# Kernel optimization log

Hardware: AMD Instinct MI355X
Metric: run time of the kernel (lower is better)

The kernel has to match this reference:

```python
import jax, jax.numpy as jnp
import numpy as np

B, Lq, C, NH, NP, DFF = 8, 10000, 256, 8, 4, 1024
H_IMG, W_IMG = 100, 100
HD = C // NH


def _layer_norm(x, g, b, eps=1e-5):
    m = jnp.mean(x, -1, keepdims=True)
    v = jnp.mean((x - m) ** 2, -1, keepdims=True)
    return (x - m) / jnp.sqrt(v + eps) * g + b


def _bilinear_sample(value, loc, Hs, Ws):
    # value: [B, Lin, NH, HD]; loc: [B, Lq, NH, NP, 2] normalized to [0,1]
    vt = jnp.transpose(value, (0, 2, 1, 3))  # [B, NH, Lin, HD]
    # move to [B, NH, Lq, NP] layout once; grid_sample(align_corners=False) pixel coords
    x = jnp.transpose(loc[..., 0], (0, 2, 1, 3)) * Ws - 0.5
    y = jnp.transpose(loc[..., 1], (0, 2, 1, 3)) * Hs - 0.5
    x0 = jnp.floor(x); y0 = jnp.floor(y)
    lx = x - x0; ly = y - y0

    def corner(xi, yi, w):
        valid = (xi >= 0) & (xi < Ws) & (yi >= 0) & (yi < Hs)
        xc = jnp.clip(xi, 0, Ws - 1).astype(jnp.int32)
        yc = jnp.clip(yi, 0, Hs - 1).astype(jnp.int32)
        idx = (yc * Ws + xc).reshape(B, NH, Lq * NP, 1)
        v = jnp.take_along_axis(vt, idx, axis=2).reshape(B, NH, Lq, NP, HD)
        return v * (w * valid)[..., None]

    acc = corner(x0, y0, (1 - lx) * (1 - ly))
    acc = acc + corner(x0 + 1, y0, lx * (1 - ly))
    acc = acc + corner(x0, y0 + 1, (1 - lx) * ly)
    acc = acc + corner(x0 + 1, y0 + 1, lx * ly)
    return acc  # [B, NH, Lq, NP, HD]


def setup_inputs() -> dict:
    key = jax.random.key(0)
    ks = jax.random.split(key, 12)
    s = 0.02
    return {
        "query": jax.random.normal(ks[0], (B, Lq, C), jnp.float32),
        "src": jax.random.normal(ks[1], (B, H_IMG * W_IMG, C), jnp.float32),
        "reference_points": jax.random.uniform(ks[2], (B, Lq, 1, 2), jnp.float32),
        "spatial_shapes": jnp.array([[H_IMG, W_IMG]], dtype=jnp.int64),
        "level_start_index": jnp.array([0], dtype=jnp.int64),
        "W_off": jax.random.normal(ks[3], (C, NH * NP * 2), jnp.float32) * s,
        "b_off": jnp.zeros((NH * NP * 2,), jnp.float32),
        "W_aw": jax.random.normal(ks[4], (C, NH * NP), jnp.float32) * s,
        "b_aw": jnp.zeros((NH * NP,), jnp.float32),
        "W_val": jax.random.normal(ks[5], (C, C), jnp.float32) * s,
        "b_val": jnp.zeros((C,), jnp.float32),
        "W_out": jax.random.normal(ks[6], (C, C), jnp.float32) * s,
        "b_out": jnp.zeros((C,), jnp.float32),
        "g1": jnp.ones((C,), jnp.float32),
        "be1": jnp.zeros((C,), jnp.float32),
        "W1": jax.random.normal(ks[7], (C, DFF), jnp.float32) * s,
        "b1": jnp.zeros((DFF,), jnp.float32),
        "W2": jax.random.normal(ks[8], (DFF, C), jnp.float32) * s,
        "b2": jnp.zeros((C,), jnp.float32),
        "g2": jnp.ones((C,), jnp.float32),
        "be2": jnp.zeros((C,), jnp.float32),
    }


def reference(query, src, reference_points, spatial_shapes, level_start_index,
              W_off, b_off, W_aw, b_aw, W_val, b_val, W_out, b_out,
              g1, be1, W1, b1, W2, b2, g2, be2):
    Hs = spatial_shapes[0, 0]
    Ws = spatial_shapes[0, 1]
    # MSDeformAttn (n_levels = 1)
    value = (src @ W_val + b_val).reshape(B, -1, NH, HD)
    off = (query @ W_off + b_off).reshape(B, Lq, NH, NP, 2)
    aw = jax.nn.softmax((query @ W_aw + b_aw).reshape(B, Lq, NH, NP), axis=-1)
    normalizer = jnp.stack([Ws, Hs]).astype(query.dtype)  # (W, H)
    loc = reference_points[:, :, None] + off / normalizer  # [B,Lq,NH,NP,2]
    sampled = _bilinear_sample(value, loc, Hs, Ws)  # [B,NH,Lq,NP,HD]
    attn = jnp.einsum('bhqpd,bqhp->bqhd', sampled, aw).reshape(B, Lq, C)
    attn = attn @ W_out + b_out
    # residual + LN + FFN + LN
    q = _layer_norm(query + attn, g1, be1)
    ffn = jax.nn.relu(q @ W1 + b1) @ W2 + b2
    return _layer_norm(q + ffn, g2, be2)
```

## Files before the change

kernel.cpp:

```cpp
#include <hip/hip_runtime.h>
#include <hip/hip_bf16.h>

typedef __hip_bfloat16 bf16;
typedef unsigned short u16;
typedef short short8 __attribute__((ext_vector_type(8)));
typedef float f32x4 __attribute__((ext_vector_type(4)));

static constexpr int B_   = 8;
static constexpr int Lq_  = 10000;
static constexpr int C_   = 256;
static constexpr int NH_  = 8;
static constexpr int NP_  = 4;
static constexpr int HIMG = 100;
static constexpr int WIMG = 100;
static constexpr int LIN  = 10000;

__device__ __forceinline__ u16 f2bf(float x) {
    union { bf16 b; u16 u; } cv; cv.b = __float2bfloat16(x); return cv.u;
}
__device__ __forceinline__ float bf2f(u16 u) {
    return __uint_as_float((unsigned)u << 16);
}

__device__ __forceinline__ void gl_lds16(const void* g, void* l) {
    __builtin_amdgcn_global_load_lds(
        (const __attribute__((address_space(1))) void*)g,
        (__attribute__((address_space(3))) void*)l, 16, 0, 0);
}
__device__ __forceinline__ void drain_barrier() {
    asm volatile("s_waitcnt vmcnt(0) lgkmcnt(0)" ::: "memory");
    __builtin_amdgcn_s_barrier();
}
#define VMW(N) asm volatile("s_waitcnt vmcnt(" #N ")" ::: "memory")
#define LKW0() asm volatile("s_waitcnt lgkmcnt(0)" ::: "memory")
#define BAR()  __builtin_amdgcn_s_barrier()

template <bool AF32, bool LN>
__global__ __launch_bounds__(512, 2) void gemm256(
    const void* __restrict__ Av, const u16* __restrict__ Bg,
    const float* __restrict__ bias, const float* __restrict__ resid,
    const float* __restrict__ gw, const float* __restrict__ bw,
    u16* __restrict__ Co, int K)
{
    __shared__ __align__(16) u16 At[2][128 * 64];
    __shared__ __align__(16) u16 Bt[2][256 * 64];
    __shared__ float red[2][128][4];

    const int tid  = threadIdx.x;
    const int lane = tid & 63;
    const int w    = tid >> 6;
    const int wm   = w >> 2, wn = w & 3;
    const int m0   = blockIdx.x * 128;

    f32x4 acc[4][4];
#pragma unroll
    for (int i = 0; i < 4; ++i)
#pragma unroll
        for (int j = 0; j < 4; ++j) acc[i][j] = f32x4{0.f, 0.f, 0.f, 0.f};

    auto stageA = [&](int t) {
        const int kt = t << 6;
        if constexpr (AF32) {
            const int row = tid >> 2;
            const int k0  = (tid & 3) << 4;
            const float* s = (const float*)Av + (size_t)(m0 + row) * K + kt + k0;
            float4 v0 = *(const float4*)(s + 0);
            float4 v1 = *(const float4*)(s + 4);
            float4 v2 = *(const float4*)(s + 8);
            float4 v3 = *(const float4*)(s + 12);
            union { short8 s8; u16 u[8]; } ga, gb;
            ga.u[0]=f2bf(v0.x); ga.u[1]=f2bf(v0.y); ga.u[2]=f2bf(v0.z); ga.u[3]=f2bf(v0.w);
            ga.u[4]=f2bf(v1.x); ga.u[5]=f2bf(v1.y); ga.u[6]=f2bf(v1.z); ga.u[7]=f2bf(v1.w);
            gb.u[0]=f2bf(v2.x); gb.u[1]=f2bf(v2.y); gb.u[2]=f2bf(v2.z); gb.u[3]=f2bf(v2.w);
            gb.u[4]=f2bf(v3.x); gb.u[5]=f2bf(v3.y); gb.u[6]=f2bf(v3.z); gb.u[7]=f2bf(v3.w);
            u16* d = &At[t & 1][row * 64];
            *(short8*)&d[(k0)     ^ ((row & 7) << 3)] = ga.s8;
            *(short8*)&d[(k0 + 8) ^ ((row & 7) << 3)] = gb.s8;
        } else {
#pragma unroll
            for (int i = 0; i < 2; ++i) {
                const int rb  = w * 16 + i * 8;
                const int row = rb + (lane >> 3);
                const int gs  = (lane & 7) ^ (row & 7);
                gl_lds16((const u16*)Av + (size_t)(m0 + row) * K + kt + gs * 8,
                         &At[t & 1][rb * 64]);
            }
        }
    };
    auto stageB = [&](int t) {
        const int kt = t << 6;
#pragma unroll
        for (int i = 0; i < 4; ++i) {
            const int rb  = w * 32 + i * 8;
            const int row = rb + (lane >> 3);
            gl_lds16(Bg + (size_t)row * K + kt + (lane & 7) * 8,
                     &Bt[t & 1][rb * 64]);
        }
    };
    auto compute = [&](int t) {
        const u16* a = At[t & 1];
        const u16* b = Bt[t & 1];
#pragma unroll
        for (int ks = 0; ks < 2; ++ks) {
            const int ko = ks * 32 + ((lane >> 4) << 3);
            short8 bfr[4];
#pragma unroll
            for (int n = 0; n < 4; ++n) {
                const int nr = wn * 64 + n * 16 + (lane & 15);
                bfr[n] = *(const short8*)&b[nr * 64 + (ko ^ ((nr & 7) << 3))];
            }
#pragma unroll
            for (int m = 0; m < 4; ++m) {
                const int ar = wm * 64 + m * 16 + (lane & 15);
                const short8 af = *(const short8*)&a[ar * 64 + (ko ^ ((ar & 7) << 3))];
#pragma unroll
                for (int n = 0; n < 4; ++n)
                    acc[m][n] = __builtin_amdgcn_mfma_f32_16x16x32_bf16(
                        af, bfr[n], acc[m][n], 0, 0, 0);
            }
        }
    };

    stageA(0); stageB(0);
    drain_barrier();
    const int nt = K >> 6;
    for (int t = 0; t < nt; ++t) {
        if (t + 1 < nt) { stageA(t + 1); stageB(t + 1); }
        compute(t);
        drain_barrier();
    }

    float bcol[4], gcol[4], becol[4];
#pragma unroll
    for (int n = 0; n < 4; ++n) {
        const int col = wn * 64 + n * 16 + (lane & 15);
        bcol[n] = bias[col];
        if (LN) { gcol[n] = gw[col]; becol[n] = bw[col]; }
    }

    if constexpr (!LN) {
#pragma unroll
        for (int m = 0; m < 4; ++m)
#pragma unroll
            for (int r = 0; r < 4; ++r) {
                const int lr = wm * 64 + m * 16 + (lane >> 4) * 4 + r;
#pragma unroll
                for (int n = 0; n < 4; ++n) {
                    const int col = wn * 64 + n * 16 + (lane & 15);
                    Co[(size_t)(m0 + lr) * 256 + col] = f2bf(acc[m][n][r] + bcol[n]);
                }
            }
    } else {
        float s[4][4], s2[4][4];
#pragma unroll
        for (int m = 0; m < 4; ++m)
#pragma unroll
            for (int r = 0; r < 4; ++r) {
                const int lr = wm * 64 + m * 16 + (lane >> 4) * 4 + r;
                float ps = 0.f, ps2 = 0.f;
#pragma unroll
                for (int n = 0; n < 4; ++n) {
                    const int col = wn * 64 + n * 16 + (lane & 15);
                    float v = acc[m][n][r] + bcol[n]
                            + resid[(size_t)(m0 + lr) * 256 + col];
                    acc[m][n][r] = v;
                    ps += v; ps2 += v * v;
                }
#pragma unroll
                for (int o = 1; o < 16; o <<= 1) {
                    ps  += __shfl_xor(ps,  o);
                    ps2 += __shfl_xor(ps2, o);
                }
                s[m][r] = ps; s2[m][r] = ps2;
            }
        if ((lane & 15) == 0) {
#pragma unroll
            for (int m = 0; m < 4; ++m)
#pragma unroll
                for (int r = 0; r < 4; ++r) {
                    const int lr = wm * 64 + m * 16 + (lane >> 4) * 4 + r;
                    red[0][lr][wn] = s[m][r];
                    red[1][lr][wn] = s2[m][r];
                }
        }
        __syncthreads();
        if (tid < 128) {
            const float ss  = red[0][tid][0] + red[0][tid][1] + red[0][tid][2] + red[0][tid][3];
            const float ss2 = red[1][tid][0] + red[1][tid][1] + red[1][tid][2] + red[1][tid][3];
            const float mean = ss * (1.f / 256.f);
            const float var  = fmaxf(ss2 * (1.f / 256.f) - mean * mean, 0.f);
            red[0][tid][0] = mean;
            red[1][tid][0] = rsqrtf(var + 1e-5f);
        }
        __syncthreads();
#pragma unroll
        for (int m = 0; m < 4; ++m)
#pragma unroll
            for (int r = 0; r < 4; ++r) {
                const int lr = wm * 64 + m * 16 + (lane >> 4) * 4 + r;
                const float mean = red[0][lr][0];
                const float rstd = red[1][lr][0];
#pragma unroll
                for (int n = 0; n < 4; ++n) {
                    const int col = wn * 64 + n * 16 + (lane & 15);
                    const float o = (acc[m][n][r] - mean) * rstd * gcol[n] + becol[n];
                    Co[(size_t)(m0 + lr) * 256 + (col ^ ((lr & 7) << 3))] = f2bf(o);
                }
            }
    }
}

__global__ __launch_bounds__(512) void ffn_fused(
    const u16* __restrict__ q1b, const u16* __restrict__ W1t,
    const u16* __restrict__ W2t, const float* __restrict__ b1,
    const float* __restrict__ b2, const float* __restrict__ g2w,
    const float* __restrict__ be2, float* __restrict__ out)
{
    __shared__ __align__(16) u16 As[128 * 256];
    __shared__ __align__(16) u16 Hs[128 * 136];
    __shared__ __align__(16) u16 B1s[3][4096];
    __shared__ __align__(16) u16 B2s[3][4096];
    float (*red)[128][4] = (float (*)[128][4])Hs;

    const int tid  = threadIdx.x;
    const int lane = tid & 63;
    const int w    = tid >> 6;
    const int wm   = w >> 2, wn = w & 3;
    const int m0   = blockIdx.x * 128;
    const int ko   = (lane >> 4) << 3;

    int bfb[2];
#pragma unroll
    for (int q = 0; q < 2; ++q) {
        const int nr = wn * 32 + q * 16 + (lane & 15);
        const int pr = nr >> 1;
        bfb[q] = pr * 64 + (nr & 1) * 32 + (ko ^ ((pr & 3) << 3));
    }
    int arow[4], aswz[4], hrow[4];
#pragma unroll
    for (int m = 0; m < 4; ++m) {
        const int ar = wm * 64 + m * 16 + (lane & 15);
        arow[m] = ar * 256; aswz[m] = (ar & 7) << 3; hrow[m] = ar * 136;
    }

    f32x4 acc2[4][4];
#pragma unroll
    for (int i = 0; i < 4; ++i)
#pragma unroll
        for (int j = 0; j < 4; ++j) acc2[i][j] = f32x4{0.f, 0.f, 0.f, 0.f};

    auto issueB1 = [&](int tile, int buf) {
        gl_lds16(W1t + (size_t)tile * 4096 + w * 512 + lane * 8, &B1s[buf][w * 512]);
    };
    auto issueB2 = [&](int tile, int buf) {
        gl_lds16(W2t + (size_t)tile * 4096 + w * 512 + lane * 8, &B2s[buf][w * 512]);
    };

#pragma unroll
    for (int i = 0; i < 8; ++i) {
        const int rb = w * 16 + i * 2;
        gl_lds16(q1b + (size_t)(m0 + rb + (lane >> 5)) * 256 + (lane & 31) * 8,
                 &As[rb * 256]);
    }
    issueB1(0, 0); issueB1(1, 1);
    VMW(1); BAR();

    for (int c = 0; c < 8; ++c) {
        const int bb = c * 8;
        f32x4 acc1[4][2];
#pragma unroll
        for (int i = 0; i < 4; ++i)
#pragma unroll
            for (int j = 0; j < 2; ++j) acc1[i][j] = f32x4{0.f, 0.f, 0.f, 0.f};

        auto g1 = [&](int t, int buf) {
            short8 bfr[2];
#pragma unroll
            for (int q = 0; q < 2; ++q)
                bfr[q] = *(const short8*)&B1s[buf][bfb[q]];
            __builtin_amdgcn_s_setprio(1);
#pragma unroll
            for (int m = 0; m < 4; ++m) {
                const short8 af = *(const short8*)
                    &As[arow[m] + ((t * 32 + ko) ^ aswz[m])];
#pragma unroll
                for (int q = 0; q < 2; ++q)
                    acc1[m][q] = __builtin_amdgcn_mfma_f32_16x16x32_bf16(
                        af, bfr[q], acc1[m][q], 0, 0, 0);
            }
            __builtin_amdgcn_s_setprio(0);
        };

#pragma unroll
        for (int t = 0; t < 6; ++t) {
            issueB1(bb + t + 2, (bb + t + 2) % 3);
            g1(t, (bb + t) % 3);
            VMW(1); BAR();
        }
        issueB2(bb + 0, (bb + 0) % 3); g1(6, (bb + 6) % 3); VMW(1); BAR();
        issueB2(bb + 1, (bb + 1) % 3); g1(7, (bb + 7) % 3); VMW(1); BAR();

#pragma unroll
        for (int q = 0; q < 2; ++q) {
            const int col = wn * 32 + q * 16 + (lane & 15);
            const float bv = b1[c * 128 + col];
#pragma unroll
            for (int m = 0; m < 4; ++m)
#pragma unroll
                for (int r = 0; r < 4; ++r) {
                    const int row = wm * 64 + m * 16 + (lane >> 4) * 4 + r;
                    Hs[row * 136 + col] = f2bf(fmaxf(acc1[m][q][r] + bv, 0.f));
                }
        }
        LKW0(); BAR();

#pragma unroll
        for (int j = 0; j < 6; ++j) {
            issueB2(bb + j + 2, (bb + j + 2) % 3);
            {
                const int ku = j >> 1, nh = j & 1;
                short8 bfr[2];
#pragma unroll
                for (int q = 0; q < 2; ++q)
                    bfr[q] = *(const short8*)&B2s[(bb + j) % 3][bfb[q]];
                __builtin_amdgcn_s_setprio(1);
#pragma unroll
                for (int m = 0; m < 4; ++m) {
                    const short8 af = *(const short8*)&Hs[hrow[m] + ku * 32 + ko];
#pragma unroll
                    for (int q = 0; q < 2; ++q)
                        acc2[m][2 * nh + q] = __builtin_amdgcn_mfma_f32_16x16x32_bf16(
                            af, bfr[q], acc2[m][2 * nh + q], 0, 0, 0);
                }
                __builtin_amdgcn_s_setprio(0);
            }
            VMW(1); BAR();
        }
#pragma unroll
        for (int j = 6; j < 8; ++j) {
            issueB1(c < 7 ? bb + 8 + (j - 6) : (j - 6), (bb + 8 + (j - 6)) % 3);
            {
                const int ku = j >> 1, nh = j & 1;
                short8 bfr[2];
#pragma unroll
                for (int q = 0; q < 2; ++q)
                    bfr[q] = *(const short8*)&B2s[(bb + j) % 3][bfb[q]];
                __builtin_amdgcn_s_setprio(1);
#pragma unroll
                for (int m = 0; m < 4; ++m) {
                    const short8 af = *(const short8*)&Hs[hrow[m] + ku * 32 + ko];
#pragma unroll
                    for (int q = 0; q < 2; ++q)
                        acc2[m][2 * nh + q] = __builtin_amdgcn_mfma_f32_16x16x32_bf16(
                            af, bfr[q], acc2[m][2 * nh + q], 0, 0, 0);
                }
                __builtin_amdgcn_s_setprio(0);
            }
            VMW(1); BAR();
        }
    }
    asm volatile("s_waitcnt vmcnt(0)" ::: "memory");
    BAR();

    float bcol[4], gcol[4], becol[4];
#pragma unroll
    for (int n = 0; n < 4; ++n) {
        const int col = wn * 64 + n * 16 + (lane & 15);
        bcol[n] = b2[col]; gcol[n] = g2w[col]; becol[n] = be2[col];
    }
    float s[4][4], s2[4][4];
#pragma unroll
    for (int m = 0; m < 4; ++m)
#pragma unroll
        for (int r = 0; r < 4; ++r) {
            const int lr = wm * 64 + m * 16 + (lane >> 4) * 4 + r;
            float ps = 0.f, ps2 = 0.f;
#pragma unroll
            for (int n = 0; n < 4; ++n) {
                const int col = wn * 64 + n * 16 + (lane & 15);
                const float q = bf2f(As[lr * 256 + (col ^ ((lr & 7) << 3))]);
                const float v = acc2[m][n][r] + bcol[n] + q;
                acc2[m][n][r] = v;
                ps += v; ps2 += v * v;
            }
#pragma unroll
            for (int o = 1; o < 16; o <<= 1) {
                ps  += __shfl_xor(ps,  o);
                ps2 += __shfl_xor(ps2, o);
            }
            s[m][r] = ps; s2[m][r] = ps2;
        }
    if ((lane & 15) == 0) {
#pragma unroll
        for (int m = 0; m < 4; ++m)
#pragma unroll
            for (int r = 0; r < 4; ++r) {
                const int lr = wm * 64 + m * 16 + (lane >> 4) * 4 + r;
                red[0][lr][wn] = s[m][r];
                red[1][lr][wn] = s2[m][r];
            }
    }
    __syncthreads();
    if (tid < 128) {
        const float ss  = red[0][tid][0] + red[0][tid][1] + red[0][tid][2] + red[0][tid][3];
        const float ss2 = red[1][tid][0] + red[1][tid][1] + red[1][tid][2] + red[1][tid][3];
        const float mean = ss * (1.f / 256.f);
        const float var  = fmaxf(ss2 * (1.f / 256.f) - mean * mean, 0.f);
        red[0][tid][0] = mean;
        red[1][tid][0] = rsqrtf(var + 1e-5f);
    }
    __syncthreads();
#pragma unroll
    for (int m = 0; m < 4; ++m)
#pragma unroll
        for (int r = 0; r < 4; ++r) {
            const int lr = wm * 64 + m * 16 + (lane >> 4) * 4 + r;
            const float mean = red[0][lr][0];
            const float rstd = red[1][lr][0];
#pragma unroll
            for (int n = 0; n < 4; ++n) {
                const int col = wn * 64 + n * 16 + (lane & 15);
                out[(size_t)(m0 + lr) * 256 + col] =
                    (acc2[m][n][r] - mean) * rstd * gcol[n] + becol[n];
            }
        }
}

__global__ __launch_bounds__(256) void gemm_oaw(
    const float* __restrict__ Av, const u16* __restrict__ Bt,
    const float* __restrict__ bias, float* __restrict__ C,
    int M, int K, int Nreal, int ldc)
{
    __shared__ __align__(16) u16 Asl[2][128 * 32];
    __shared__ __align__(16) u16 Bsl[2][128 * 32];

    const int tid  = threadIdx.x;
    const int lane = tid & 63;
    const int w    = tid >> 6;
    const int wr   = (w >> 1) * 64;
    const int wc   = (w & 1) * 64;
    const int m0   = blockIdx.y * 128;
    const int n0   = blockIdx.x * 128;

    const int srow = lane >> 2;
    const int scol = (lane & 3) << 3;
    const u16* bG = Bt + (size_t)(n0 + w * 32 + srow) * K + scol;
    const size_t rstep16 = (size_t)16 * K;

    const int ar  = lane >> 3;
    const int ac  = (lane & 7) << 2;
    const float* aGf = Av + (size_t)(m0 + w * 32 + ar) * K + ac;

    const int aRoff = (wr + (lane & 15)) * 32 + (lane >> 4) * 8;
    const int bRoff = (wc + (lane & 15)) * 32 + (lane >> 4) * 8;

    f32x4 acc[4][4];
#pragma unroll
    for (int i = 0; i < 4; ++i)
#pragma unroll
        for (int j = 0; j < 4; ++j) acc[i][j] = f32x4{0.f, 0.f, 0.f, 0.f};

    float4 a4[4];
    const int nt = K >> 5;

#pragma unroll
    for (int rep = 0; rep < 4; ++rep)
        a4[rep] = *(const float4*)(aGf + (size_t)(rep * 8) * K);
#pragma unroll
    for (int rep = 0; rep < 4; ++rep) {
        ushort4 v{f2bf(a4[rep].x), f2bf(a4[rep].y), f2bf(a4[rep].z), f2bf(a4[rep].w)};
        *(ushort4*)&Asl[0][(w * 32 + rep * 8 + ar) * 32 + ac] = v;
    }
    gl_lds16(bG, &Bsl[0][(w * 32) * 32]);
    gl_lds16(bG + rstep16, &Bsl[0][(w * 32 + 16) * 32]);
    drain_barrier();

    for (int t = 0; t < nt; ++t) {
        const int cur = t & 1, nxt = cur ^ 1;
        const int k0n = (t + 1) << 5;
        const bool has_next = (t + 1 < nt);
        if (has_next) {
#pragma unroll
            for (int rep = 0; rep < 4; ++rep)
                a4[rep] = *(const float4*)(aGf + k0n + (size_t)(rep * 8) * K);
            gl_lds16(bG + k0n, &Bsl[nxt][(w * 32) * 32]);
            gl_lds16(bG + k0n + rstep16, &Bsl[nxt][(w * 32 + 16) * 32]);
        }
        short8 af[4], bfr[4];
#pragma unroll
        for (int m = 0; m < 4; ++m) af[m]  = *(const short8*)&Asl[cur][aRoff + m * 16 * 32];
#pragma unroll
        for (int n = 0; n < 4; ++n) bfr[n] = *(const short8*)&Bsl[cur][bRoff + n * 16 * 32];
#pragma unroll
        for (int m = 0; m < 4; ++m)
#pragma unroll
            for (int n = 0; n < 4; ++n)
                acc[m][n] = __builtin_amdgcn_mfma_f32_16x16x32_bf16(
                    af[m], bfr[n], acc[m][n], 0, 0, 0);
        if (has_next) {
#pragma unroll
            for (int rep = 0; rep < 4; ++rep) {
                ushort4 v{f2bf(a4[rep].x), f2bf(a4[rep].y), f2bf(a4[rep].z), f2bf(a4[rep].w)};
                *(ushort4*)&Asl[nxt][(w * 32 + rep * 8 + ar) * 32 + ac] = v;
            }
        }
        drain_barrier();
    }

#pragma unroll
    for (int n = 0; n < 4; ++n) {
        const int gc = n0 + wc + n * 16 + (lane & 15);
        if (gc >= Nreal) continue;
        const float bv = bias[gc];
        const int gr0 = m0 + wr + (lane >> 4) * 4;
#pragma unroll
        for (int m = 0; m < 4; ++m)
#pragma unroll
            for (int r = 0; r < 4; ++r)
                C[(size_t)(gr0 + m * 16 + r) * ldc + gc] = acc[m][n][r] + bv;
    }
}

__global__ __launch_bounds__(256) void prep_all(
    const float* __restrict__ Wv, const float* __restrict__ Wo,
    const float* __restrict__ W1, const float* __restrict__ W2,
    const float* __restrict__ Woff, const float* __restrict__ Waw,
    const float* __restrict__ boff, const float* __restrict__ baw,
    u16* __restrict__ Wvs, u16* __restrict__ Wos,
    u16* __restrict__ W1t, u16* __restrict__ W2t,
    u16* __restrict__ Woa, float* __restrict__ boa)
{
    const int idx = blockIdx.x * 256 + threadIdx.x;
    if (idx < 65536) {
        const int n = idx >> 8, kd = idx & 255;
        Wvs[idx] = f2bf(Wv[(size_t)(kd ^ ((n & 7) << 3)) * 256 + n]);
    } else if (idx < 131072) {
        const int i = idx - 65536, n = i >> 8, kd = i & 255;
        Wos[i] = f2bf(Wo[(size_t)(kd ^ ((n & 7) << 3)) * 256 + n]);
    } else if (idx < 393216) {
        const int i = idx - 131072;
        const int tile = i >> 12, si = i & 4095;
        const int c = tile >> 3, t = tile & 7;
        const int pr = si >> 6, inner = si & 63;
        const int nr = (pr << 1) | (inner >> 5);
        const int kk = (inner & 31) ^ ((pr & 3) << 3);
        W1t[i] = f2bf(W1[(size_t)(t * 32 + kk) * 1024 + c * 128 + nr]);
    } else if (idx < 655360) {
        const int i = idx - 393216;
        const int tile = i >> 12, si = i & 4095;
        const int c = tile >> 3, j = tile & 7;
        const int ku = j >> 1, nh = j & 1;
        const int pr = si >> 6, inner = si & 63;
        const int rl = (pr << 1) | (inner >> 5);
        const int kk = (inner & 31) ^ ((pr & 3) << 3);
        const int n = ((rl >> 5) << 6) + (nh << 5) + (rl & 31);
        W2t[i] = f2bf(W2[(size_t)(c * 128 + ku * 32 + kk) * 256 + n]);
    } else if (idx < 688128) {
        const int i = idx - 655360, n = i >> 8, k = i & 255;
        float v = 0.f;
        if (n < 64)      v = Woff[(size_t)k * 64 + n];
        else if (n < 96) v = Waw[(size_t)k * 32 + (n - 64)];
        Woa[i] = f2bf(v);
    } else if (idx < 688256) {
        const int i = idx - 688128;
        boa[i] = (i < 64) ? boff[i] : (i < 96 ? baw[i - 64] : 0.f);
    }
}

__global__ __launch_bounds__(256) void sample_attn(
    const u16* __restrict__ val, const float* __restrict__ oaw,
    const float* __restrict__ refp, u16* __restrict__ attn)
{
    const int t   = threadIdx.x;
    const int gid = blockIdx.x * 64 + (t >> 2);
    const int c0  = (t & 3) << 3;
    const int h   = gid & (NH_ - 1);
    const int bq  = gid >> 3;

    const float* row = oaw + (size_t)bq * 96;
    const float rx = refp[(size_t)bq * 2 + 0] * (float)WIMG;
    const float ry = refp[(size_t)bq * 2 + 1] * (float)HIMG;

    const float4 aw4 = *(const float4*)(row + 64 + h * 4);
    const float mx = fmaxf(fmaxf(aw4.x, aw4.y), fmaxf(aw4.z, aw4.w));
    const float e0 = __expf(aw4.x - mx), e1 = __expf(aw4.y - mx);
    const float e2 = __expf(aw4.z - mx), e3 = __expf(aw4.w - mx);
    const float inv = 1.f / (e0 + e1 + e2 + e3);
    const float w4[4] = {e0 * inv, e1 * inv, e2 * inv, e3 * inv};

    const int b = bq / Lq_;
    const u16* vb = val + (size_t)b * LIN * C_ + h * 32 + c0;

    float acc[8] = {};
#pragma unroll
    for (int p = 0; p < NP_; ++p) {
        const float2 off = *(const float2*)(row + (h * 4 + p) * 2);
        const float x = rx + off.x - 0.5f;
        const float y = ry + off.y - 0.5f;
        const float xf = floorf(x), yf = floorf(y);
        const float lx = x - xf, ly = y - yf;
        const int x0 = (int)xf, y0 = (int)yf;
        const float wp = w4[p];
        const float w00 = wp * (1.f - lx) * (1.f - ly);
        const float w10 = wp * lx * (1.f - ly);
        const float w01 = wp * (1.f - lx) * ly;
        const float w11 = wp * lx * ly;

#pragma unroll
        for (int c = 0; c < 4; ++c) {
            const int xi = x0 + (c & 1);
            const int yi = y0 + (c >> 1);
            const float wc = (c == 0) ? w00 : (c == 1) ? w10 : (c == 2) ? w01 : w11;
            const bool v = ((unsigned)xi < (unsigned)WIMG) & ((unsigned)yi < (unsigned)HIMG);
            const int idx = v ? (yi * WIMG + xi) : 0;
            const float w = v ? wc : 0.f;
            const short8 d = *(const short8*)(vb + (size_t)idx * C_);
#pragma unroll
            for (int j = 0; j < 8; ++j)
                acc[j] = fmaf(w, bf2f(((const u16*)&d)[j]), acc[j]);
        }
    }

    union { short8 s; u16 u[8]; } o;
#pragma unroll
    for (int j = 0; j < 8; ++j) o.u[j] = f2bf(acc[j]);
    *(short8*)(attn + (size_t)bq * C_ + h * 32 + c0) = o.s;
}

extern "C" void kernel_launch(void* const* d_in, const int* in_sizes, int n_in,
                              void* d_out, int out_size, void* d_ws, size_t ws_size,
                              hipStream_t stream)
{
    const float* query = (const float*)d_in[0];
    const float* src   = (const float*)d_in[1];
    const float* refp  = (const float*)d_in[2];
    const float* W_off = (const float*)d_in[5];
    const float* b_off = (const float*)d_in[6];
    const float* W_aw  = (const float*)d_in[7];
    const float* b_aw  = (const float*)d_in[8];
    const float* W_val = (const float*)d_in[9];
    const float* b_val = (const float*)d_in[10];
    const float* W_out = (const float*)d_in[11];
    const float* b_out = (const float*)d_in[12];
    const float* g1    = (const float*)d_in[13];
    const float* be1   = (const float*)d_in[14];
    const float* W1    = (const float*)d_in[15];
    const float* b1    = (const float*)d_in[16];
    const float* W2    = (const float*)d_in[17];
    const float* b2    = (const float*)d_in[18];
    const float* g2    = (const float*)d_in[19];
    const float* be2   = (const float*)d_in[20];
    float* out = (float*)d_out;

    char* ws = (char*)d_ws;
    const int R = B_ * Lq_;

    u16*  val  = (u16*)(ws + 0);
    float* oaw = (float*)(ws + 40960000);
    u16*  attn = (u16*)(ws + 71680000);
    u16*  q1b  = (u16*)(ws + 112640000);
    u16*  Wvs  = (u16*)(ws + 153600000);
    u16*  Wos  = (u16*)(ws + 153600000 + 131072);
    u16*  W1t  = (u16*)(ws + 153600000 + 262144);
    u16*  W2t  = (u16*)(ws + 153600000 + 786432);
    u16*  Woa  = (u16*)(ws + 153600000 + 1310720);
    float* boa = (float*)(ws + 153600000 + 1376256);

    prep_all<<<2689, 256, 0, stream>>>(W_val, W_out, W1, W2, W_off, W_aw,
                                       b_off, b_aw, Wvs, Wos, W1t, W2t,
                                       Woa, boa);

    gemm256<true, false><<<625, 512, 0, stream>>>(
        src, Wvs, b_val, nullptr, nullptr, nullptr, val, 256);

    gemm_oaw<<<dim3(1, 625), 256, 0, stream>>>(
        query, Woa, boa, oaw, R, 256, 96, 96);

    sample_attn<<<10000, 256, 0, stream>>>(val, oaw, refp, attn);

    gemm256<false, true><<<625, 512, 0, stream>>>(
        attn, Wos, b_out, query, g1, be1, q1b, 256);

    ffn_fused<<<625, 512, 0, stream>>>(q1b, W1t, W2t, b1, b2, g2, be2, out);
}
```

Baseline: 374.3 us.

## Retile fused FFN to 64-row blocks with double-buffered weight staging

The fused FFN kernel moves from 128-row tiles with 512 threads to 64-row tiles with 256 threads, launched as 1250 blocks. The triple-buffered, partially waited weight pipeline becomes a double buffer with a full drain barrier after each k-step. The hidden tile gets an XOR swizzle in place of padding, and the W2 prepack layout changes to match the new per-wave column split. Shared-memory use drops so more blocks can fit on a CU and the 1250 blocks spread more evenly across CUs. In exchange, each weight tile is fetched twice as often per output row, the load/compute overlap is coarser, and the MFMA priority hints are gone.

```diff
diff --git a/kernel.cpp b/kernel.cpp
--- a/kernel.cpp
+++ b/kernel.cpp
@@ -31,9 +31,6 @@
     asm volatile("s_waitcnt vmcnt(0) lgkmcnt(0)" ::: "memory");
     __builtin_amdgcn_s_barrier();
 }
-#define VMW(N) asm volatile("s_waitcnt vmcnt(" #N ")" ::: "memory")
-#define LKW0() asm volatile("s_waitcnt lgkmcnt(0)" ::: "memory")
-#define BAR()  __builtin_amdgcn_s_barrier()
 
 template <bool AF32, bool LN>
 __global__ __launch_bounds__(512, 2) void gemm256(
@@ -210,50 +207,57 @@
     }
 }
 
-__global__ __launch_bounds__(512) void ffn_fused(
+__global__ __launch_bounds__(256) void ffn_fused(
     const u16* __restrict__ q1b, const u16* __restrict__ W1t,
     const u16* __restrict__ W2t, const float* __restrict__ b1,
     const float* __restrict__ b2, const float* __restrict__ g2w,
     const float* __restrict__ be2, float* __restrict__ out)
 {
-    __shared__ __align__(16) u16 As[128 * 256];
-    __shared__ __align__(16) u16 Hs[128 * 136];
-    __shared__ __align__(16) u16 B1s[3][4096];
-    __shared__ __align__(16) u16 B2s[3][4096];
-    float (*red)[128][4] = (float (*)[128][4])Hs;
+    __shared__ __align__(16) u16 As[64 * 256];
+    __shared__ __align__(16) u16 Hs[64 * 128];
+    __shared__ __align__(16) u16 B1s[2][4096];
+    __shared__ __align__(16) u16 B2s[2][4096];
+    float (*red)[64][2] = (float (*)[64][2])Hs;
 
     const int tid  = threadIdx.x;
     const int lane = tid & 63;
     const int w    = tid >> 6;
-    const int wm   = w >> 2, wn = w & 3;
-    const int m0   = blockIdx.x * 128;
+    const int wm   = w >> 1, wn = w & 1;
+    const int m0   = blockIdx.x * 64;
     const int ko   = (lane >> 4) << 3;
 
-    int bfb[2];
-#pragma unroll
-    for (int q = 0; q < 2; ++q) {
-        const int nr = wn * 32 + q * 16 + (lane & 15);
+    int bfb[4];
+#pragma unroll
+    for (int q = 0; q < 4; ++q) {
+        const int nr = wn * 64 + q * 16 + (lane & 15);
         const int pr = nr >> 1;
         bfb[q] = pr * 64 + (nr & 1) * 32 + (ko ^ ((pr & 3) << 3));
     }
-    int arow[4], aswz[4], hrow[4];
-#pragma unroll
-    for (int m = 0; m < 4; ++m) {
-        const int ar = wm * 64 + m * 16 + (lane & 15);
-        arow[m] = ar * 256; aswz[m] = (ar & 7) << 3; hrow[m] = ar * 136;
-    }
-
-    f32x4 acc2[4][4];
-#pragma unroll
-    for (int i = 0; i < 4; ++i)
-#pragma unroll
-        for (int j = 0; j < 4; ++j) acc2[i][j] = f32x4{0.f, 0.f, 0.f, 0.f};
-
-    auto issueB1 = [&](int tile, int buf) {
-        gl_lds16(W1t + (size_t)tile * 4096 + w * 512 + lane * 8, &B1s[buf][w * 512]);
+    int arow[2], aswz[2], hrow[2], hswz[2];
+#pragma unroll
+    for (int m = 0; m < 2; ++m) {
+        const int ar = wm * 32 + m * 16 + (lane & 15);
+        arow[m] = ar * 256; aswz[m] = (ar & 7) << 3;
+        hrow[m] = ar * 128; hswz[m] = (ar & 7) << 3;
+    }
+
+    f32x4 acc2[2][8];
+#pragma unroll
+    for (int i = 0; i < 2; ++i)
+#pragma unroll
+        for (int j = 0; j < 8; ++j) acc2[i][j] = f32x4{0.f, 0.f, 0.f, 0.f};
+
+    auto stageB1 = [&](int tile, int buf) {
+#pragma unroll
+        for (int i = 0; i < 2; ++i)
+            gl_lds16(W1t + (size_t)tile * 4096 + w * 1024 + i * 512 + lane * 8,
+                     &B1s[buf][w * 1024 + i * 512]);
     };
-    auto issueB2 = [&](int tile, int buf) {
-        gl_lds16(W2t + (size_t)tile * 4096 + w * 512 + lane * 8, &B2s[buf][w * 512]);
+    auto stageB2 = [&](int tile, int buf) {
+#pragma unroll
+        for (int i = 0; i < 2; ++i)
+            gl_lds16(W2t + (size_t)tile * 4096 + w * 1024 + i * 512 + lane * 8,
+                     &B2s[buf][w * 1024 + i * 512]);
     };
 
 #pragma unroll
@@ -262,125 +266,92 @@
         gl_lds16(q1b + (size_t)(m0 + rb + (lane >> 5)) * 256 + (lane & 31) * 8,
                  &As[rb * 256]);
     }
-    issueB1(0, 0); issueB1(1, 1);
-    VMW(1); BAR();
+    stageB1(0, 0);
+    drain_barrier();
 
     for (int c = 0; c < 8; ++c) {
-        const int bb = c * 8;
-        f32x4 acc1[4][2];
-#pragma unroll
-        for (int i = 0; i < 4; ++i)
-#pragma unroll
-            for (int j = 0; j < 2; ++j) acc1[i][j] = f32x4{0.f, 0.f, 0.f, 0.f};
-
-        auto g1 = [&](int t, int buf) {
-            short8 bfr[2];
-#pragma unroll
-            for (int q = 0; q < 2; ++q)
-                bfr[q] = *(const short8*)&B1s[buf][bfb[q]];
-            __builtin_amdgcn_s_setprio(1);
-#pragma unroll
-            for (int m = 0; m < 4; ++m) {
+        f32x4 acc1[2][4];
+#pragma unroll
+        for (int i = 0; i < 2; ++i)
+#pragma unroll
+            for (int j = 0; j < 4; ++j) acc1[i][j] = f32x4{0.f, 0.f, 0.f, 0.f};
+
+#pragma unroll
+        for (int t = 0; t < 8; ++t) {
+            if (t < 7) stageB1(c * 8 + t + 1, (t + 1) & 1);
+            else       stageB2(c * 8 + 0, 0);
+            short8 bfr[4];
+#pragma unroll
+            for (int q = 0; q < 4; ++q)
+                bfr[q] = *(const short8*)&B1s[t & 1][bfb[q]];
+#pragma unroll
+            for (int m = 0; m < 2; ++m) {
                 const short8 af = *(const short8*)
                     &As[arow[m] + ((t * 32 + ko) ^ aswz[m])];
 #pragma unroll
-                for (int q = 0; q < 2; ++q)
+                for (int q = 0; q < 4; ++q)
                     acc1[m][q] = __builtin_amdgcn_mfma_f32_16x16x32_bf16(
                         af, bfr[q], acc1[m][q], 0, 0, 0);
             }
-            __builtin_amdgcn_s_setprio(0);
-        };
-
-#pragma unroll
-        for (int t = 0; t < 6; ++t) {
-            issueB1(bb + t + 2, (bb + t + 2) % 3);
-            g1(t, (bb + t) % 3);
-            VMW(1); BAR();
-        }
-        issueB2(bb + 0, (bb + 0) % 3); g1(6, (bb + 6) % 3); VMW(1); BAR();
-        issueB2(bb + 1, (bb + 1) % 3); g1(7, (bb + 7) % 3); VMW(1); BAR();
-
-#pragma unroll
-        for (int q = 0; q < 2; ++q) {
-            const int col = wn * 32 + q * 16 + (lane & 15);
+            drain_barrier();
+        }
+
+#pragma unroll
+        for (int q = 0; q < 4; ++q) {
+            const int col = wn * 64 + q * 16 + (lane & 15);
             const float bv = b1[c * 128 + col];
 #pragma unroll
-            for (int m = 0; m < 4; ++m)
+            for (int m = 0; m < 2; ++m)
 #pragma unroll
                 for (int r = 0; r < 4; ++r) {
-                    const int row = wm * 64 + m * 16 + (lane >> 4) * 4 + r;
-                    Hs[row * 136 + col] = f2bf(fmaxf(acc1[m][q][r] + bv, 0.f));
+                    const int row = wm * 32 + m * 16 + (lane >> 4) * 4 + r;
+                    Hs[row * 128 + (col ^ ((row & 7) << 3))] =
+                        f2bf(fmaxf(acc1[m][q][r] + bv, 0.f));
                 }
         }
-        LKW0(); BAR();
-
-#pragma unroll
-        for (int j = 0; j < 6; ++j) {
-            issueB2(bb + j + 2, (bb + j + 2) % 3);
-            {
-                const int ku = j >> 1, nh = j & 1;
-                short8 bfr[2];
-#pragma unroll
-                for (int q = 0; q < 2; ++q)
-                    bfr[q] = *(const short8*)&B2s[(bb + j) % 3][bfb[q]];
-                __builtin_amdgcn_s_setprio(1);
-#pragma unroll
-                for (int m = 0; m < 4; ++m) {
-                    const short8 af = *(const short8*)&Hs[hrow[m] + ku * 32 + ko];
-#pragma unroll
-                    for (int q = 0; q < 2; ++q)
-                        acc2[m][2 * nh + q] = __builtin_amdgcn_mfma_f32_16x16x32_bf16(
-                            af, bfr[q], acc2[m][2 * nh + q], 0, 0, 0);
-                }
-                __builtin_amdgcn_s_setprio(0);
-            }
-            VMW(1); BAR();
-        }
-#pragma unroll
-        for (int j = 6; j < 8; ++j) {
-            issueB1(c < 7 ? bb + 8 + (j - 6) : (j - 6), (bb + 8 + (j - 6)) % 3);
-            {
-                const int ku = j >> 1, nh = j & 1;
-                short8 bfr[2];
-#pragma unroll
-                for (int q = 0; q < 2; ++q)
-                    bfr[q] = *(const short8*)&B2s[(bb + j) % 3][bfb[q]];
-                __builtin_amdgcn_s_setprio(1);
-#pragma unroll
-                for (int m = 0; m < 4; ++m) {
-                    const short8 af = *(const short8*)&Hs[hrow[m] + ku * 32 + ko];
-#pragma unroll
-                    for (int q = 0; q < 2; ++q)
-                        acc2[m][2 * nh + q] = __builtin_amdgcn_mfma_f32_16x16x32_bf16(
-                            af, bfr[q], acc2[m][2 * nh + q], 0, 0, 0);
-                }
-                __builtin_amdgcn_s_setprio(0);
-            }
-            VMW(1); BAR();
-        }
-    }
-    asm volatile("s_waitcnt vmcnt(0)" ::: "memory");
-    BAR();
-
-    float bcol[4], gcol[4], becol[4];
-#pragma unroll
-    for (int n = 0; n < 4; ++n) {
-        const int col = wn * 64 + n * 16 + (lane & 15);
-        bcol[n] = b2[col]; gcol[n] = g2w[col]; becol[n] = be2[col];
-    }
-    float s[4][4], s2[4][4];
-#pragma unroll
-    for (int m = 0; m < 4; ++m)
+        drain_barrier();
+
+#pragma unroll
+        for (int j = 0; j < 8; ++j) {
+            if (j < 7) stageB2(c * 8 + j + 1, (j + 1) & 1);
+            else       stageB1(c < 7 ? (c + 1) * 8 : 0, 0);
+            const int ku = j >> 1, nh = j & 1;
+            short8 bfr[4];
+#pragma unroll
+            for (int q = 0; q < 4; ++q)
+                bfr[q] = *(const short8*)&B2s[j & 1][bfb[q]];
+#pragma unroll
+            for (int m = 0; m < 2; ++m) {
+                const short8 af = *(const short8*)
+                    &Hs[hrow[m] + ((ku * 32 + ko) ^ hswz[m])];
+#pragma unroll
+                for (int q = 0; q < 4; ++q)
+                    acc2[m][nh * 4 + q] = __builtin_amdgcn_mfma_f32_16x16x32_bf16(
+                        af, bfr[q], acc2[m][nh * 4 + q], 0, 0, 0);
+            }
+            drain_barrier();
+        }
+    }
+
+    float bcol[8], gcol[8], becol[8];
+#pragma unroll
+    for (int nf = 0; nf < 8; ++nf) {
+        const int col = (nf >> 2) * 128 + wn * 64 + (nf & 3) * 16 + (lane & 15);
+        bcol[nf] = b2[col]; gcol[nf] = g2w[col]; becol[nf] = be2[col];
+    }
+    float s[2][4], s2[2][4];
+#pragma unroll
+    for (int m = 0; m < 2; ++m)
 #pragma unroll
         for (int r = 0; r < 4; ++r) {
-            const int lr = wm * 64 + m * 16 + (lane >> 4) * 4 + r;
+            const int lr = wm * 32 + m * 16 + (lane >> 4) * 4 + r;
             float ps = 0.f, ps2 = 0.f;
 #pragma unroll
-            for (int n = 0; n < 4; ++n) {
-                const int col = wn * 64 + n * 16 + (lane & 15);
+            for (int nf = 0; nf < 8; ++nf) {
+                const int col = (nf >> 2) * 128 + wn * 64 + (nf & 3) * 16 + (lane & 15);
                 const float q = bf2f(As[lr * 256 + (col ^ ((lr & 7) << 3))]);
-                const float v = acc2[m][n][r] + bcol[n] + q;
-                acc2[m][n][r] = v;
+                const float v = acc2[m][nf][r] + bcol[nf] + q;
+                acc2[m][nf][r] = v;
                 ps += v; ps2 += v * v;
             }
 #pragma unroll
@@ -392,18 +363,18 @@
         }
     if ((lane & 15) == 0) {
 #pragma unroll
-        for (int m = 0; m < 4; ++m)
+        for (int m = 0; m < 2; ++m)
 #pragma unroll
             for (int r = 0; r < 4; ++r) {
-                const int lr = wm * 64 + m * 16 + (lane >> 4) * 4 + r;
+                const int lr = wm * 32 + m * 16 + (lane >> 4) * 4 + r;
                 red[0][lr][wn] = s[m][r];
                 red[1][lr][wn] = s2[m][r];
             }
     }
     __syncthreads();
-    if (tid < 128) {
-        const float ss  = red[0][tid][0] + red[0][tid][1] + red[0][tid][2] + red[0][tid][3];
-        const float ss2 = red[1][tid][0] + red[1][tid][1] + red[1][tid][2] + red[1][tid][3];
+    if (tid < 64) {
+        const float ss  = red[0][tid][0] + red[0][tid][1];
+        const float ss2 = red[1][tid][0] + red[1][tid][1];
         const float mean = ss * (1.f / 256.f);
         const float var  = fmaxf(ss2 * (1.f / 256.f) - mean * mean, 0.f);
         red[0][tid][0] = mean;
@@ -411,17 +382,17 @@
     }
     __syncthreads();
 #pragma unroll
-    for (int m = 0; m < 4; ++m)
+    for (int m = 0; m < 2; ++m)
 #pragma unroll
         for (int r = 0; r < 4; ++r) {
-            const int lr = wm * 64 + m * 16 + (lane >> 4) * 4 + r;
+            const int lr = wm * 32 + m * 16 + (lane >> 4) * 4 + r;
             const float mean = red[0][lr][0];
             const float rstd = red[1][lr][0];
 #pragma unroll
-            for (int n = 0; n < 4; ++n) {
-                const int col = wn * 64 + n * 16 + (lane & 15);
+            for (int nf = 0; nf < 8; ++nf) {
+                const int col = (nf >> 2) * 128 + wn * 64 + (nf & 3) * 16 + (lane & 15);
                 out[(size_t)(m0 + lr) * 256 + col] =
-                    (acc2[m][n][r] - mean) * rstd * gcol[n] + becol[n];
+                    (acc2[m][nf][r] - mean) * rstd * gcol[nf] + becol[nf];
             }
         }
 }
@@ -553,7 +524,7 @@
         const int pr = si >> 6, inner = si & 63;
         const int rl = (pr << 1) | (inner >> 5);
         const int kk = (inner & 31) ^ ((pr & 3) << 3);
-        const int n = ((rl >> 5) << 6) + (nh << 5) + (rl & 31);
+        const int n = (nh << 7) + rl;
         W2t[i] = f2bf(W2[(size_t)(c * 128 + ku * 32 + kk) * 256 + n]);
     } else if (idx < 688128) {
         const int i = idx - 655360, n = i >> 8, k = i & 255;
@@ -681,5 +652,5 @@
     gemm256<false, true><<<625, 512, 0, stream>>>(
         attn, Wos, b_out, query, g1, be1, q1b, 256);
 
-    ffn_fused<<<625, 512, 0, stream>>>(q1b, W1t, W2t, b1, b2, g2, be2, out);
-}
+    ffn_fused<<<1250, 256, 0, stream>>>(q1b, W1t, W2t, b1, b2, g2, be2, out);
+}
```

Measured after the change: 440.0 us. 1.18x slower.

## Restream FFN A-operand in K-chunks and double-buffer larger weight tiles

Applied to the files above, without the earlier changes.

The fused FFN kernel no longer keeps the full 128x256 input row-block in LDS. It streams 64-wide K slices of the input, re-reading them from global memory for each of the 8 hidden chunks. Weight tiles are repacked into larger 64-K (W1) and full-256-N (W2) tiles with double buffering and full drain barriers instead of a triple-buffered vmcnt(1) pipeline. The aim is to shrink the LDS footprint so occupancy rises, and to cut barrier count with larger per-step MFMA work. The trade-offs are 8x more global/L2 traffic for the input, full vmcnt(0) drains that expose load latency, and residual reads from global in the epilogue.

```diff
diff --git a/kernel.cpp b/kernel.cpp
--- a/kernel.cpp
+++ b/kernel.cpp
@@ -31,7 +31,6 @@
     asm volatile("s_waitcnt vmcnt(0) lgkmcnt(0)" ::: "memory");
     __builtin_amdgcn_s_barrier();
 }
-#define VMW(N) asm volatile("s_waitcnt vmcnt(" #N ")" ::: "memory")
 #define LKW0() asm volatile("s_waitcnt lgkmcnt(0)" ::: "memory")
 #define BAR()  __builtin_amdgcn_s_barrier()
 
@@ -211,15 +210,15 @@
 }
 
 __global__ __launch_bounds__(512) void ffn_fused(
-    const u16* __restrict__ q1b, const u16* __restrict__ W1t,
-    const u16* __restrict__ W2t, const float* __restrict__ b1,
+    const u16* __restrict__ q1b, const u16* __restrict__ W1f,
+    const u16* __restrict__ W2f, const float* __restrict__ b1,
     const float* __restrict__ b2, const float* __restrict__ g2w,
     const float* __restrict__ be2, float* __restrict__ out)
 {
-    __shared__ __align__(16) u16 As[128 * 256];
+    __shared__ __align__(16) u16 Asl[2][128 * 64];
     __shared__ __align__(16) u16 Hs[128 * 136];
-    __shared__ __align__(16) u16 B1s[3][4096];
-    __shared__ __align__(16) u16 B2s[3][4096];
+    __shared__ __align__(16) u16 B1s[2][128 * 64];
+    __shared__ __align__(16) u16 B2s[2][256 * 32];
     float (*red)[128][4] = (float (*)[128][4])Hs;
 
     const int tid  = threadIdx.x;
@@ -229,18 +228,24 @@
     const int m0   = blockIdx.x * 128;
     const int ko   = (lane >> 4) << 3;
 
-    int bfb[2];
+    int arow[4], aswz[4], hrow[4];
+#pragma unroll
+    for (int m = 0; m < 4; ++m) {
+        const int ar = wm * 64 + m * 16 + (lane & 15);
+        arow[m] = ar * 64; aswz[m] = (ar & 7) << 3; hrow[m] = ar * 136;
+    }
+    int b1r[2], b1x[2];
 #pragma unroll
     for (int q = 0; q < 2; ++q) {
         const int nr = wn * 32 + q * 16 + (lane & 15);
+        b1r[q] = nr * 64; b1x[q] = (nr & 7) << 3;
+    }
+    int b2i[4];
+#pragma unroll
+    for (int q = 0; q < 4; ++q) {
+        const int nr = wn * 64 + q * 16 + (lane & 15);
         const int pr = nr >> 1;
-        bfb[q] = pr * 64 + (nr & 1) * 32 + (ko ^ ((pr & 3) << 3));
-    }
-    int arow[4], aswz[4], hrow[4];
-#pragma unroll
-    for (int m = 0; m < 4; ++m) {
-        const int ar = wm * 64 + m * 16 + (lane & 15);
-        arow[m] = ar * 256; aswz[m] = (ar & 7) << 3; hrow[m] = ar * 136;
+        b2i[q] = pr * 64 + (nr & 1) * 32 + (ko ^ ((pr & 3) << 3));
     }
 
     f32x4 acc2[4][4];
@@ -249,56 +254,81 @@
 #pragma unroll
         for (int j = 0; j < 4; ++j) acc2[i][j] = f32x4{0.f, 0.f, 0.f, 0.f};
 
-    auto issueB1 = [&](int tile, int buf) {
-        gl_lds16(W1t + (size_t)tile * 4096 + w * 512 + lane * 8, &B1s[buf][w * 512]);
+    auto stageAs = [&](int t, int buf) {
+#pragma unroll
+        for (int i = 0; i < 2; ++i) {
+            const int rb = w * 16 + i * 8;
+            gl_lds16(q1b + (size_t)(m0 + rb + (lane >> 3)) * 256 + t * 64 + (lane & 7) * 8,
+                     &Asl[buf][rb * 64]);
+        }
     };
-    auto issueB2 = [&](int tile, int buf) {
-        gl_lds16(W2t + (size_t)tile * 4096 + w * 512 + lane * 8, &B2s[buf][w * 512]);
+    auto stageB1 = [&](int c, int t, int buf) {
+#pragma unroll
+        for (int i = 0; i < 2; ++i)
+            gl_lds16(W1f + (size_t)(c * 4 + t) * 8192 + w * 1024 + i * 512 + lane * 8,
+                     &B1s[buf][w * 1024 + i * 512]);
     };
-
-#pragma unroll
-    for (int i = 0; i < 8; ++i) {
-        const int rb = w * 16 + i * 2;
-        gl_lds16(q1b + (size_t)(m0 + rb + (lane >> 5)) * 256 + (lane & 31) * 8,
-                 &As[rb * 256]);
-    }
-    issueB1(0, 0); issueB1(1, 1);
-    VMW(1); BAR();
+    auto stageB2 = [&](int c, int u, int buf) {
+#pragma unroll
+        for (int i = 0; i < 2; ++i)
+            gl_lds16(W2f + (size_t)(c * 4 + u) * 8192 + w * 1024 + i * 512 + lane * 8,
+                     &B2s[buf][w * 1024 + i * 512]);
+    };
+
+    stageAs(0, 0); stageB1(0, 0, 0);
+    drain_barrier();
 
     for (int c = 0; c < 8; ++c) {
-        const int bb = c * 8;
         f32x4 acc1[4][2];
 #pragma unroll
         for (int i = 0; i < 4; ++i)
 #pragma unroll
             for (int j = 0; j < 2; ++j) acc1[i][j] = f32x4{0.f, 0.f, 0.f, 0.f};
 
-        auto g1 = [&](int t, int buf) {
-            short8 bfr[2];
-#pragma unroll
-            for (int q = 0; q < 2; ++q)
-                bfr[q] = *(const short8*)&B1s[buf][bfb[q]];
+        auto g1 = [&](int t) {
+            const u16* a = Asl[t & 1];
+            const u16* b = B1s[t & 1];
             __builtin_amdgcn_s_setprio(1);
 #pragma unroll
-            for (int m = 0; m < 4; ++m) {
-                const short8 af = *(const short8*)
-                    &As[arow[m] + ((t * 32 + ko) ^ aswz[m])];
+            for (int ks = 0; ks < 2; ++ks) {
+                const int kk = ks * 32 + ko;
+                short8 bfr[2];
 #pragma unroll
                 for (int q = 0; q < 2; ++q)
-                    acc1[m][q] = __builtin_amdgcn_mfma_f32_16x16x32_bf16(
-                        af, bfr[q], acc1[m][q], 0, 0, 0);
+                    bfr[q] = *(const short8*)&b[b1r[q] + (kk ^ b1x[q])];
+#pragma unroll
+                for (int m = 0; m < 4; ++m) {
+                    const short8 af = *(const short8*)&a[arow[m] + (kk ^ aswz[m])];
+#pragma unroll
+                    for (int q = 0; q < 2; ++q)
+                        acc1[m][q] = __builtin_amdgcn_mfma_f32_16x16x32_bf16(
+                            af, bfr[q], acc1[m][q], 0, 0, 0);
+                }
             }
             __builtin_amdgcn_s_setprio(0);
         };
-
-#pragma unroll
-        for (int t = 0; t < 6; ++t) {
-            issueB1(bb + t + 2, (bb + t + 2) % 3);
-            g1(t, (bb + t) % 3);
-            VMW(1); BAR();
-        }
-        issueB2(bb + 0, (bb + 0) % 3); g1(6, (bb + 6) % 3); VMW(1); BAR();
-        issueB2(bb + 1, (bb + 1) % 3); g1(7, (bb + 7) % 3); VMW(1); BAR();
+        auto g2 = [&](int u) {
+            const u16* b = B2s[u & 1];
+            __builtin_amdgcn_s_setprio(1);
+            short8 bfr[4];
+#pragma unroll
+            for (int q = 0; q < 4; ++q)
+                bfr[q] = *(const short8*)&b[b2i[q]];
+#pragma unroll
+            for (int m = 0; m < 4; ++m) {
+                const short8 af = *(const short8*)&Hs[hrow[m] + u * 32 + ko];
+#pragma unroll
+                for (int q = 0; q < 4; ++q)
+                    acc2[m][q] = __builtin_amdgcn_mfma_f32_16x16x32_bf16(
+                        af, bfr[q], acc2[m][q], 0, 0, 0);
+            }
+            __builtin_amdgcn_s_setprio(0);
+        };
+
+        stageAs(1, 1); stageB1(c, 1, 1);                   g1(0); drain_barrier();
+        stageAs(2, 0); stageB1(c, 2, 0);                   g1(1); drain_barrier();
+        stageAs(3, 1); stageB1(c, 3, 1); stageB2(c, 0, 0); g1(2); drain_barrier();
+        stageB2(c, 1, 1);                                  g1(3); drain_barrier();
 
 #pragma unroll
         for (int q = 0; q < 2; ++q) {
@@ -314,53 +344,12 @@
         }
         LKW0(); BAR();
 
-#pragma unroll
-        for (int j = 0; j < 6; ++j) {
-            issueB2(bb + j + 2, (bb + j + 2) % 3);
-            {
-                const int ku = j >> 1, nh = j & 1;
-                short8 bfr[2];
-#pragma unroll
-                for (int q = 0; q < 2; ++q)
-                    bfr[q] = *(const short8*)&B2s[(bb + j) % 3][bfb[q]];
-                __builtin_amdgcn_s_setprio(1);
-#pragma unroll
-                for (int m = 0; m < 4; ++m) {
-                    const short8 af = *(const short8*)&Hs[hrow[m] + ku * 32 + ko];
-#pragma unroll
-                    for (int q = 0; q < 2; ++q)
-                        acc2[m][2 * nh + q] = __builtin_amdgcn_mfma_f32_16x16x32_bf16(
-                            af, bfr[q], acc2[m][2 * nh + q], 0, 0, 0);
-                }
-                __builtin_amdgcn_s_setprio(0);
-            }
-            VMW(1); BAR();
-        }
-#pragma unroll
-        for (int j = 6; j < 8; ++j) {
-            issueB1(c < 7 ? bb + 8 + (j - 6) : (j - 6), (bb + 8 + (j - 6)) % 3);
-            {
-                const int ku = j >> 1, nh = j & 1;
-                short8 bfr[2];
-#pragma unroll
-                for (int q = 0; q < 2; ++q)
-                    bfr[q] = *(const short8*)&B2s[(bb + j) % 3][bfb[q]];
-                __builtin_amdgcn_s_setprio(1);
-#pragma unroll
-                for (int m = 0; m < 4; ++m) {
-                    const short8 af = *(const short8*)&Hs[hrow[m] + ku * 32 + ko];
-#pragma unroll
-                    for (int q = 0; q < 2; ++q)
-                        acc2[m][2 * nh + q] = __builtin_amdgcn_mfma_f32_16x16x32_bf16(
-                            af, bfr[q], acc2[m][2 * nh + q], 0, 0, 0);
-                }
-                __builtin_amdgcn_s_setprio(0);
-            }
-            VMW(1); BAR();
-        }
-    }
-    asm volatile("s_waitcnt vmcnt(0)" ::: "memory");
-    BAR();
+        g2(0); drain_barrier();
+        stageB2(c, 2, 0);                                  g2(1); drain_barrier();
+        if (c < 7) { stageAs(0, 0); stageB1(c + 1, 0, 0); }
+        stageB2(c, 3, 1);                                  g2(2); drain_barrier();
+        g2(3); drain_barrier();
+    }
 
     float bcol[4], gcol[4], becol[4];
 #pragma unroll
@@ -378,7 +367,7 @@
 #pragma unroll
             for (int n = 0; n < 4; ++n) {
                 const int col = wn * 64 + n * 16 + (lane & 15);
-                const float q = bf2f(As[lr * 256 + (col ^ ((lr & 7) << 3))]);
+                const float q = bf2f(q1b[(size_t)(m0 + lr) * 256 + (col ^ ((lr & 7) << 3))]);
                 const float v = acc2[m][n][r] + bcol[n] + q;
                 acc2[m][n][r] = v;
                 ps += v; ps2 += v * v;
@@ -527,7 +516,7 @@
     const float* __restrict__ Woff, const float* __restrict__ Waw,
     const float* __restrict__ boff, const float* __restrict__ baw,
     u16* __restrict__ Wvs, u16* __restrict__ Wos,
-    u16* __restrict__ W1t, u16* __restrict__ W2t,
+    u16* __restrict__ W1f, u16* __restrict__ W2f,
     u16* __restrict__ Woa, float* __restrict__ boa)
 {
     const int idx = blockIdx.x * 256 + threadIdx.x;
@@ -539,22 +528,17 @@
         Wos[i] = f2bf(Wo[(size_t)(kd ^ ((n & 7) << 3)) * 256 + n]);
     } else if (idx < 393216) {
         const int i = idx - 131072;
-        const int tile = i >> 12, si = i & 4095;
-        const int c = tile >> 3, t = tile & 7;
-        const int pr = si >> 6, inner = si & 63;
-        const int nr = (pr << 1) | (inner >> 5);
-        const int kk = (inner & 31) ^ ((pr & 3) << 3);
-        W1t[i] = f2bf(W1[(size_t)(t * 32 + kk) * 1024 + c * 128 + nr]);
+        const int tile = i >> 13, si = i & 8191;
+        const int c = tile >> 2, t = tile & 3;
+        const int n = si >> 6, kd = si & 63;
+        W1f[i] = f2bf(W1[(size_t)(t * 64 + (kd ^ ((n & 7) << 3))) * 1024 + c * 128 + n]);
     } else if (idx < 655360) {
         const int i = idx - 393216;
-        const int tile = i >> 12, si = i & 4095;
-        const int c = tile >> 3, j = tile & 7;
-        const int ku = j >> 1, nh = j & 1;
-        const int pr = si >> 6, inner = si & 63;
-        const int rl = (pr << 1) | (inner >> 5);
-        const int kk = (inner & 31) ^ ((pr & 3) << 3);
-        const int n = ((rl >> 5) << 6) + (nh << 5) + (rl & 31);
-        W2t[i] = f2bf(W2[(size_t)(c * 128 + ku * 32 + kk) * 256 + n]);
+        const int tile = i >> 13, si = i & 8191;
+        const int c = tile >> 2, u = tile & 3;
+        const int pr = si >> 6, h = (si >> 5) & 1, e = si & 31;
+        const int n = (pr << 1) | h;
+        W2f[i] = f2bf(W2[(size_t)(c * 128 + u * 32 + (e ^ ((pr & 3) << 3))) * 256 + n]);
     } else if (idx < 688128) {
         const int i = idx - 655360, n = i >> 8, k = i & 255;
         float v = 0.f;
@@ -661,13 +645,13 @@
     u16*  q1b  = (u16*)(ws + 112640000);
     u16*  Wvs  = (u16*)(ws + 153600000);
     u16*  Wos  = (u16*)(ws + 153600000 + 131072);
-    u16*  W1t  = (u16*)(ws + 153600000 + 262144);
-    u16*  W2t  = (u16*)(ws + 153600000 + 786432);
+    u16*  W1f  = (u16*)(ws + 153600000 + 262144);
+    u16*  W2f  = (u16*)(ws + 153600000 + 786432);
     u16*  Woa  = (u16*)(ws + 153600000 + 1310720);
     float* boa = (float*)(ws + 153600000 + 1376256);
 
     prep_all<<<2689, 256, 0, stream>>>(W_val, W_out, W1, W2, W_off, W_aw,
-                                       b_off, b_aw, Wvs, Wos, W1t, W2t,
+                                       b_off, b_aw, Wvs, Wos, W1f, W2f,
                                        Woa, boa);
 
     gemm256<true, false><<<625, 512, 0, stream>>>(
@@ -681,5 +665,5 @@
     gemm256<false, true><<<625, 512, 0, stream>>>(
         attn, Wos, b_out, query, g1, be1, q1b, 256);
 
-    ffn_fused<<<625, 512, 0, stream>>>(q1b, W1t, W2t, b1, b2, g2, be2, out);
-}
+    ffn_fused<<<625, 512, 0, stream>>>(q1b, W1f, W2f, b1, b2, g2, be2, out);
+}
```

New measurement: 333.7 us. -10.8%, faster.
